# Kernel optimization log

Measured on AMD Instinct MI355X. Metric: run time of the kernel, lower is better.

Reference implementation:

```python
import jax, jax.numpy as jnp
import numpy as np

BETA = 0.5
THRESHOLD = 1e-12
NORM_EPS = 1e-12
SQRT_EPS = 1e-12


def _l2_normalize(x):
    # matches torch F.normalize(p=2, dim=1, eps=1e-12): x / max(||x||, eps)
    n = jnp.sqrt(jnp.sum(x * x, axis=1, keepdims=True))
    return x / jnp.maximum(n, NORM_EPS)


def _focal(d):
    # reg_method='log': log(beta*d + 1) if d > threshold else 0
    d_safe = jnp.where(d > THRESHOLD, d, THRESHOLD)
    return jnp.where(d > THRESHOLD, jnp.log(BETA * d_safe + 1.0), 0.0)


def setup_inputs() -> dict:
    key = jax.random.key(0)
    ks = jax.random.split(key, 6)
    B, D = 128, 512
    return {
        "x_audio": jax.random.normal(ks[0], (B, D), dtype=jnp.float32),
        "x_video": jax.random.normal(ks[1], (B, D), dtype=jnp.float32),
        "x_text": jax.random.normal(ks[2], (B, D), dtype=jnp.float32),
        "loss_audio": jax.random.uniform(ks[3], (), dtype=jnp.float32),
        "loss_video": jax.random.uniform(ks[4], (), dtype=jnp.float32),
        "loss_text": jax.random.uniform(ks[5], (), dtype=jnp.float32),
    }


def reference(x_audio, x_video, x_text, loss_audio, loss_video, loss_text):
    xs = [x_audio, x_video, x_text]
    losses = [loss_audio, loss_video, loss_text]
    R = len(xs)
    # L2-normalize each modality, then per-sample outer-product correlations [B, D, D]
    corr = [jnp.einsum('bi,bj->bij', xn, xn)
            for xn in (_l2_normalize(x) for x in xs)]
    ssa = []
    for m in range(R):
        acc = jnp.float32(0.0)
        for n in range(R):
            focal = _focal(losses[m] - losses[n])
            diff = corr[m] - corr[n]
            corr_diff = jnp.sqrt(SQRT_EPS + jnp.sum(diff * diff))
            acc = acc + focal * corr_diff
        ssa.append(acc)
    return jnp.stack(ssa)  # [R] ssa loss per modality
```

## Files before the change

kernel.cpp:

```cpp
#include <hip/hip_runtime.h>
#include <math.h>


#define SSA_BETA      0.5f
#define SSA_THRESHOLD 1e-12f
#define SSA_NORM_EPS  1e-12f
#define SSA_SQRT_EPS  1e-12f

static constexpr int SSA_B = 128;
static constexpr int SSA_D = 512;

__global__ __launch_bounds__(64) void ssa_rows_kernel(
    const float* __restrict__ xa, const float* __restrict__ xv,
    const float* __restrict__ xt, float* __restrict__ ws) {
  const int b = blockIdx.x;
  const int lane = threadIdx.x;

  const float4* pa = reinterpret_cast<const float4*>(xa + b * SSA_D);
  const float4* pv = reinterpret_cast<const float4*>(xv + b * SSA_D);
  const float4* pt = reinterpret_cast<const float4*>(xt + b * SSA_D);

  float sa = 0.f, sv = 0.f, st = 0.f;
  float dav = 0.f, dat = 0.f, dvt = 0.f;

#pragma unroll
  for (int k = 0; k < 2; ++k) {
    const int idx = lane + 64 * k;
    const float4 a = pa[idx];
    const float4 v = pv[idx];
    const float4 t = pt[idx];
    sa  += a.x * a.x + a.y * a.y + a.z * a.z + a.w * a.w;
    sv  += v.x * v.x + v.y * v.y + v.z * v.z + v.w * v.w;
    st  += t.x * t.x + t.y * t.y + t.z * t.z + t.w * t.w;
    dav += a.x * v.x + a.y * v.y + a.z * v.z + a.w * v.w;
    dat += a.x * t.x + a.y * t.y + a.z * t.z + a.w * t.w;
    dvt += v.x * t.x + v.y * t.y + v.z * t.z + v.w * t.w;
  }

#pragma unroll
  for (int off = 32; off > 0; off >>= 1) {
    sa  += __shfl_xor(sa, off);
    sv  += __shfl_xor(sv, off);
    st  += __shfl_xor(st, off);
    dav += __shfl_xor(dav, off);
    dat += __shfl_xor(dat, off);
    dvt += __shfl_xor(dvt, off);
  }

  if (lane == 0) {
    const float na = fmaxf(sqrtf(sa), SSA_NORM_EPS);
    const float nv = fmaxf(sqrtf(sv), SSA_NORM_EPS);
    const float nt = fmaxf(sqrtf(st), SSA_NORM_EPS);
    const float na2 = sa / (na * na);
    const float nv2 = sv / (nv * nv);
    const float nt2 = st / (nt * nt);
    const float cav = dav / (na * nv);
    const float cat_ = dat / (na * nt);
    const float cvt_ = dvt / (nv * nt);
    ws[0 * SSA_B + b] = na2 * na2 + nv2 * nv2 - 2.f * cav * cav;
    ws[1 * SSA_B + b] = na2 * na2 + nt2 * nt2 - 2.f * cat_ * cat_;
    ws[2 * SSA_B + b] = nv2 * nv2 + nt2 * nt2 - 2.f * cvt_ * cvt_;
  }
}

__global__ __launch_bounds__(128) void ssa_final_kernel(
    const float* __restrict__ ws, const float* __restrict__ la,
    const float* __restrict__ lv, const float* __restrict__ lt,
    float* __restrict__ out) {
  const int tid = threadIdx.x;
  float s0 = ws[0 * SSA_B + tid];
  float s1 = ws[1 * SSA_B + tid];
  float s2 = ws[2 * SSA_B + tid];

#pragma unroll
  for (int off = 32; off > 0; off >>= 1) {
    s0 += __shfl_xor(s0, off);
    s1 += __shfl_xor(s1, off);
    s2 += __shfl_xor(s2, off);
  }

  __shared__ float sm[3][2];
  const int wave = tid >> 6;
  if ((tid & 63) == 0) {
    sm[0][wave] = s0;
    sm[1][wave] = s1;
    sm[2][wave] = s2;
  }
  __syncthreads();

  if (tid == 0) {
    const float S01 = sm[0][0] + sm[0][1];
    const float S02 = sm[1][0] + sm[1][1];
    const float S12 = sm[2][0] + sm[2][1];

    const float dist01 = sqrtf(SSA_SQRT_EPS + S01);
    const float dist02 = sqrtf(SSA_SQRT_EPS + S02);
    const float dist12 = sqrtf(SSA_SQRT_EPS + S12);

    const float loss[3] = {la[0], lv[0], lt[0]};
    const float dist[3][3] = {{0.f, dist01, dist02},
                              {dist01, 0.f, dist12},
                              {dist02, dist12, 0.f}};
#pragma unroll
    for (int m = 0; m < 3; ++m) {
      float acc = 0.f;
#pragma unroll
      for (int n = 0; n < 3; ++n) {
        if (n == m) continue;
        const float d = loss[m] - loss[n];
        const float focal = (d > SSA_THRESHOLD) ? logf(SSA_BETA * d + 1.0f) : 0.f;
        acc += focal * dist[m][n];
      }
      out[m] = acc;
    }
  }
}

extern "C" void kernel_launch(void* const* d_in, const int* in_sizes, int n_in,
                              void* d_out, int out_size, void* d_ws, size_t ws_size,
                              hipStream_t stream) {
  const float* xa = (const float*)d_in[0];
  const float* xv = (const float*)d_in[1];
  const float* xt = (const float*)d_in[2];
  const float* la = (const float*)d_in[3];
  const float* lv = (const float*)d_in[4];
  const float* lt = (const float*)d_in[5];
  float* out = (float*)d_out;
  float* ws = (float*)d_ws;

  ssa_rows_kernel<<<SSA_B, 64, 0, stream>>>(xa, xv, xt, ws);
  ssa_final_kernel<<<1, 128, 0, stream>>>(ws, la, lv, lt, out);
}
```

Before: 11.42 us.

## Fuse row and final reduction kernels via last-block atomic counter

Merges the per-row kernel and the single-block final reduction into one launch. Each block writes its partials, fences, and bumps an atomic counter in workspace; the block that sees the counter reach 127 mod 128 does the final reduction and writes the outputs. This removes one kernel launch and the gap between kernels, at the cost of an atomic, memory fences, and a counter that relies on never being reset (the modulo handles repeated calls only if the workspace is not cleared to a non-multiple).

Result: no change. 11.53 us (+1.0%).

```diff
diff --git a/kernel.cpp b/kernel.cpp
--- a/kernel.cpp
+++ b/kernel.cpp
@@ -9,10 +9,13 @@
 
 static constexpr int SSA_B = 128;
 static constexpr int SSA_D = 512;
+static constexpr int SSA_CTR_OFS = 512;
 
-__global__ __launch_bounds__(64) void ssa_rows_kernel(
+__global__ __launch_bounds__(64) void ssa_fused_kernel(
     const float* __restrict__ xa, const float* __restrict__ xv,
-    const float* __restrict__ xt, float* __restrict__ ws) {
+    const float* __restrict__ xt, const float* __restrict__ la,
+    const float* __restrict__ lv, const float* __restrict__ lt,
+    float* __restrict__ out, float* __restrict__ ws) {
   const int b = blockIdx.x;
   const int lane = threadIdx.x;
 
@@ -54,23 +57,28 @@
     const float na2 = sa / (na * na);
     const float nv2 = sv / (nv * nv);
     const float nt2 = st / (nt * nt);
-    const float cav = dav / (na * nv);
+    const float cav  = dav / (na * nv);
     const float cat_ = dat / (na * nt);
     const float cvt_ = dvt / (nv * nt);
-    ws[0 * SSA_B + b] = na2 * na2 + nv2 * nv2 - 2.f * cav * cav;
+    ws[0 * SSA_B + b] = na2 * na2 + nv2 * nv2 - 2.f * cav  * cav;
     ws[1 * SSA_B + b] = na2 * na2 + nt2 * nt2 - 2.f * cat_ * cat_;
     ws[2 * SSA_B + b] = nv2 * nv2 + nt2 * nt2 - 2.f * cvt_ * cvt_;
   }
-}
 
-__global__ __launch_bounds__(128) void ssa_final_kernel(
-    const float* __restrict__ ws, const float* __restrict__ la,
-    const float* __restrict__ lv, const float* __restrict__ lt,
-    float* __restrict__ out) {
-  const int tid = threadIdx.x;
-  float s0 = ws[0 * SSA_B + tid];
-  float s1 = ws[1 * SSA_B + tid];
-  float s2 = ws[2 * SSA_B + tid];
+  __threadfence();
+
+  unsigned int old = 0;
+  if (lane == 0) {
+    old = atomicAdd(reinterpret_cast<unsigned int*>(ws + SSA_CTR_OFS), 1u);
+  }
+  old = __shfl(old, 0);
+  if ((old & 127u) != 127u) return;
+
+  __threadfence();
+
+  float s0 = ws[0 * SSA_B + lane] + ws[0 * SSA_B + lane + 64];
+  float s1 = ws[1 * SSA_B + lane] + ws[1 * SSA_B + lane + 64];
+  float s2 = ws[2 * SSA_B + lane] + ws[2 * SSA_B + lane + 64];
 
 #pragma unroll
   for (int off = 32; off > 0; off >>= 1) {
@@ -79,23 +87,10 @@
     s2 += __shfl_xor(s2, off);
   }
 
-  __shared__ float sm[3][2];
-  const int wave = tid >> 6;
-  if ((tid & 63) == 0) {
-    sm[0][wave] = s0;
-    sm[1][wave] = s1;
-    sm[2][wave] = s2;
-  }
-  __syncthreads();
-
-  if (tid == 0) {
-    const float S01 = sm[0][0] + sm[0][1];
-    const float S02 = sm[1][0] + sm[1][1];
-    const float S12 = sm[2][0] + sm[2][1];
-
-    const float dist01 = sqrtf(SSA_SQRT_EPS + S01);
-    const float dist02 = sqrtf(SSA_SQRT_EPS + S02);
-    const float dist12 = sqrtf(SSA_SQRT_EPS + S12);
+  if (lane == 0) {
+    const float dist01 = sqrtf(SSA_SQRT_EPS + s0);
+    const float dist02 = sqrtf(SSA_SQRT_EPS + s1);
+    const float dist12 = sqrtf(SSA_SQRT_EPS + s2);
 
     const float loss[3] = {la[0], lv[0], lt[0]};
     const float dist[3][3] = {{0.f, dist01, dist02},
@@ -128,6 +123,5 @@
   float* out = (float*)d_out;
   float* ws = (float*)d_ws;
 
-  ssa_rows_kernel<<<SSA_B, 64, 0, stream>>>(xa, xv, xt, ws);
-  ssa_final_kernel<<<1, 128, 0, stream>>>(ws, la, lv, lt, out);
+  ssa_fused_kernel<<<SSA_B, 64, 0, stream>>>(xa, xv, xt, la, lv, lt, out, ws);
 }
```
